# Kernel optimization log

Measured on AMD Instinct MI355X. Metric: run time of the kernel, lower is better.

## Reference

```python
import jax, jax.numpy as jnp
import numpy as np


def setup_inputs() -> dict:
    key = jax.random.key(0)
    k1, k2, k3, k4 = jax.random.split(key, 4)
    B, S, D_IN, D_OUT = 8, 2048, 4096, 4096
    inputs = jax.random.normal(k1, (B, S, D_IN), dtype=jnp.float32)
    # int8-valued weights stored as int32 (same math; original stores torch.int8)
    int8_weights = jax.random.randint(k2, (D_OUT, D_IN), -127, 128, dtype=jnp.int32)
    # realistic per-row dequant scales (small positive)
    scales = jax.random.uniform(k3, (D_OUT,), dtype=jnp.float32, minval=0.001, maxval=0.02)
    bias = jax.random.normal(k4, (1, D_OUT), dtype=jnp.float32) * 0.01
    return {"inputs": inputs, "int8_weights": int8_weights, "scales": scales, "bias": bias}


def reference(inputs, int8_weights, scales, bias):
    # converted_weights = int8_weights.to(inputs.dtype); F.linear(inputs, W) = inputs @ W.T
    w = int8_weights.astype(inputs.dtype)                      # [out, in]
    out = jnp.einsum('bsi,oi->bso', inputs, w)                 # [B, S, out]
    out = out * scales                                         # per-output-row scale
    out = out + bias                                           # bias broadcast [1, out]
    return out
```

## Files before the change

kernel.cpp:

```cpp
#include <hip/hip_runtime.h>
#include <hip/hip_bf16.h>

#define M_TOTAL 16384
#define N_TOTAL 4096
#define K_TOTAL 4096
#define NT (K_TOTAL / 128)

typedef __attribute__((ext_vector_type(4))) int i32x4;
typedef __attribute__((ext_vector_type(4))) float f32x4;

__device__ __forceinline__ unsigned pack4(int a, int b, int c, int d) {
  return (a & 0xFF) | ((b & 0xFF) << 8) | ((c & 0xFF) << 16) | ((d & 0xFF) << 24);
}

__global__ __launch_bounds__(256) void quant_a(const float* __restrict__ A,
                                               unsigned* __restrict__ Aq,
                                               float* __restrict__ ascale) {
  const int row = blockIdx.x;
  const int tid = threadIdx.x;
  const float4* src = reinterpret_cast<const float4*>(A + (size_t)row * K_TOTAL);
  float4 v[4];
#pragma unroll
  for (int c = 0; c < 4; ++c) v[c] = src[tid + 256 * c];
  float amax = 0.0f;
#pragma unroll
  for (int c = 0; c < 4; ++c) {
    amax = fmaxf(amax, fmaxf(fmaxf(fabsf(v[c].x), fabsf(v[c].y)),
                             fmaxf(fabsf(v[c].z), fabsf(v[c].w))));
  }
#pragma unroll
  for (int off = 32; off > 0; off >>= 1) amax = fmaxf(amax, __shfl_xor(amax, off, 64));
  __shared__ float wmax[4];
  if ((tid & 63) == 0) wmax[tid >> 6] = amax;
  __syncthreads();
  amax = fmaxf(fmaxf(wmax[0], wmax[1]), fmaxf(wmax[2], wmax[3]));
  amax = fmaxf(amax, 1e-20f);
  const float rs = 127.0f / amax;
  if (tid == 0) ascale[row] = amax * (1.0f / 127.0f);

  unsigned* dst = Aq + (size_t)row * (K_TOTAL / 4);
#pragma unroll
  for (int c = 0; c < 4; ++c) {
    int q[4];
    float f[4] = {v[c].x, v[c].y, v[c].z, v[c].w};
#pragma unroll
    for (int i = 0; i < 4; ++i) {
      int t = (int)rintf(f[i] * rs);
      q[i] = t < -127 ? -127 : (t > 127 ? 127 : t);
    }
    dst[tid + 256 * c] = pack4(q[0], q[1], q[2], q[3]);
  }
}

__global__ void cvt_w_i8(const int* __restrict__ W, unsigned* __restrict__ Wq, int n4) {
  const int stride = gridDim.x * blockDim.x;
  for (int i = blockIdx.x * blockDim.x + threadIdx.x; i < n4; i += stride) {
    int4 v = reinterpret_cast<const int4*>(W)[i];
    Wq[i] = pack4(v.x, v.y, v.z, v.w);
  }
}

#define GLOAD_LDS16(gp, lp)                                                \
  __builtin_amdgcn_global_load_lds(                                        \
      (const __attribute__((address_space(1))) void*)(gp),                 \
      (__attribute__((address_space(3))) void*)(lp), 16, 0, 0)

#define BAR() asm volatile("s_barrier" ::: "memory")
#define VM(n) asm volatile("s_waitcnt vmcnt(" #n ")" ::: "memory")


__global__ __launch_bounds__(512, 2) void w8a16_gemm_i8(
    const signed char* __restrict__ A,
    const signed char* __restrict__ Bt,
    const float* __restrict__ ascale,
    const float* __restrict__ scales, const float* __restrict__ bias,
    float* __restrict__ C) {
  __shared__ alignas(16) unsigned char lds[131072];

  const int tid = threadIdx.x;
  const int w = tid >> 6, l = tid & 63;
  const int wr = w >> 2, wc = w & 3;

  const int bid = blockIdx.x;
  const int swz = ((bid & 7) << 7) + (bid >> 3);
  const int bn = swz & 15, bm = swz >> 4;

  const int rowq = tid >> 3;
  const int colb = ((l & 7) ^ (l >> 3)) << 4;
  const signed char* pA = A + (size_t)(bm * 256 + rowq) * K_TOTAL + colb;
  const signed char* pB = Bt + (size_t)(bn * 256 + rowq) * K_TOTAL + colb;
  unsigned char* const ldsp = lds;
  const int woff = w << 10;

#define SDA(b_, h_) (ldsp + (b_) * 65536 + (h_) * 16384 + woff)
#define SDB(b_, h_) (ldsp + (b_) * 65536 + 32768 + (h_) * 16384 + woff)
#define STAGE_A(b_, h_, t_)                                                    \
  do {                                                                         \
    GLOAD_LDS16(pA + (size_t)((h_) * 128) * K_TOTAL + (t_) * 128, SDA(b_, h_));\
    GLOAD_LDS16(pA + (size_t)((h_) * 128 + 64) * K_TOTAL + (t_) * 128,         \
                SDA(b_, h_) + 8192);                                           \
  } while (0)
#define STAGE_B(b_, h_, t_)                                                    \
  do {                                                                         \
    GLOAD_LDS16(pB + (size_t)((h_) * 128) * K_TOTAL + (t_) * 128, SDB(b_, h_));\
    GLOAD_LDS16(pB + (size_t)((h_) * 128 + 64) * K_TOTAL + (t_) * 128,         \
                SDB(b_, h_) + 8192);                                           \
  } while (0)

  const int arow = ((l & 15) << 7) + ((((l >> 4) ^ (l & 7)) & 7) << 4);

  i32x4 af[8];
  i32x4 bfr[8];
  i32x4 acc[8][4] = {{}};

#define RD_A(mh_)                                                             \
  do {                                                                        \
    const unsigned char* Ab_ = ldsp + bsel * 65536 + wr * 16384;              \
    _Pragma("unroll") for (int fm = 0; fm < 4; ++fm)                          \
        _Pragma("unroll") for (int kk = 0; kk < 2; ++kk)                      \
            af[fm * 2 + kk] = *(const i32x4*)(Ab_ + ((mh_) * 4 + fm) * 2048 + \
                                              (arow ^ (kk << 6)));            \
  } while (0)
#define RD_B(nh_)                                                             \
  do {                                                                        \
    const unsigned char* Bb_ = ldsp + bsel * 65536 + 32768 +                  \
                               (wc >> 1) * 16384 + (wc & 1) * 8192;           \
    _Pragma("unroll") for (int fn = 0; fn < 2; ++fn)                          \
        _Pragma("unroll") for (int kk = 0; kk < 2; ++kk)                      \
            bfr[((nh_) * 2 + fn) * 2 + kk] =                                  \
                *(const i32x4*)(Bb_ + ((nh_) * 2 + fn) * 2048 +               \
                                (arow ^ (kk << 6)));                          \
  } while (0)
#define QUAD(mh_, nh_)                                                        \
  do {                                                                        \
    __builtin_amdgcn_s_setprio(1);                                            \
    _Pragma("unroll") for (int m = 0; m < 4; ++m)                             \
        _Pragma("unroll") for (int n = 0; n < 2; ++n)                         \
            _Pragma("unroll") for (int kk = 0; kk < 2; ++kk)                  \
                acc[(mh_) * 4 + m][(nh_) * 2 + n] =                           \
                    __builtin_amdgcn_mfma_i32_16x16x64_i8(                    \
                        af[m * 2 + kk], bfr[((nh_) * 2 + n) * 2 + kk],        \
                        acc[(mh_) * 4 + m][(nh_) * 2 + n], 0, 0, 0);          \
    __builtin_amdgcn_s_setprio(0);                                            \
  } while (0)

  STAGE_A(0, 0, 0); STAGE_A(0, 1, 0);
  STAGE_B(0, 0, 0); STAGE_B(0, 1, 0);
  STAGE_B(1, 0, 1); STAGE_B(1, 1, 1);
  STAGE_A(1, 0, 1);
  VM(6);
  BAR();

  for (int t = 0; t < NT; ++t) {
    const int bsel = t & 1;
    RD_A(0); RD_B(0);
    if (t + 1 < NT) STAGE_A(bsel ^ 1, 1, t + 1);
    BAR();
    QUAD(0, 0);
    BAR();
    RD_B(1);
    if (t + 2 < NT) STAGE_B(bsel, 0, t + 2);
    BAR();
    QUAD(0, 1);
    BAR();
    RD_A(1);
    if (t + 2 < NT) STAGE_B(bsel, 1, t + 2);
    BAR();
    QUAD(1, 1);
    BAR();
    if (t + 2 < NT) STAGE_A(bsel, 0, t + 2);
    BAR();
    QUAD(1, 0);
    if (t < NT - 2) { VM(6); } else { VM(0); }
    BAR();
  }

  const int row0 = bm * 256 + wr * 128 + ((l >> 4) << 2);
  const int col0 = bn * 256 + wc * 64 + (l & 15);
#pragma unroll
  for (int fn = 0; fn < 4; ++fn) {
    const int col = col0 + fn * 16;
    const float sc = scales[col];
    const float bi = bias[col];
#pragma unroll
    for (int fm = 0; fm < 8; ++fm) {
      const int r = row0 + fm * 16;
      float* cp = C + (size_t)r * N_TOTAL + col;
#pragma unroll
      for (int j = 0; j < 4; ++j)
        cp[(size_t)j * N_TOTAL] = fmaf((float)acc[fm][fn][j], ascale[r + j] * sc, bi);
    }
  }
}

__global__ void naive_gemm(const float* __restrict__ A, const int* __restrict__ W,
                           const float* __restrict__ scales, const float* __restrict__ bias,
                           float* __restrict__ C) {
  size_t idx = (size_t)blockIdx.x * blockDim.x + threadIdx.x;
  if (idx >= (size_t)M_TOTAL * N_TOTAL) return;
  const int n = (int)(idx % N_TOTAL);
  const size_t m = idx / N_TOTAL;
  const float* a = A + m * (size_t)K_TOTAL;
  const int* w = W + (size_t)n * K_TOTAL;
  float s = 0.f;
  for (int k = 0; k < K_TOTAL; ++k) s = fmaf(a[k], (float)w[k], s);
  C[idx] = fmaf(s, scales[n], bias[n]);
}

extern "C" void kernel_launch(void* const* d_in, const int* in_sizes, int n_in,
                              void* d_out, int out_size, void* d_ws, size_t ws_size,
                              hipStream_t stream) {
  const float* A = (const float*)d_in[0];
  const int* W = (const int*)d_in[1];
  const float* scales = (const float*)d_in[2];
  const float* bias = (const float*)d_in[3];
  float* out = (float*)d_out;

  const size_t a_elems = (size_t)M_TOTAL * K_TOTAL;
  const size_t w_elems = (size_t)N_TOTAL * K_TOTAL;
  const size_t need = a_elems + w_elems + (size_t)M_TOTAL * sizeof(float);

  if (ws_size >= need) {
    signed char* A_q = (signed char*)d_ws;
    signed char* W_q = A_q + a_elems;
    float* a_s = (float*)(W_q + w_elems);
    quant_a<<<M_TOTAL, 256, 0, stream>>>(A, (unsigned*)A_q, a_s);
    cvt_w_i8<<<2048, 256, 0, stream>>>(W, (unsigned*)W_q, (int)(w_elems / 4));
    w8a16_gemm_i8<<<1024, 512, 0, stream>>>(A_q, W_q, a_s, scales, bias, out);
  } else {
    size_t total = (size_t)M_TOTAL * N_TOTAL;
    naive_gemm<<<(unsigned)((total + 255) / 256), 256, 0, stream>>>(A, W, scales, bias, out);
  }
}
```

Baseline: 380.9 us.

## Load B fragments directly from global into registers, bypassing LDS

The weight (B) tile no longer goes through LDS. Each wave loads its own B fragments straight from global memory into registers, issued at the end of each k-step for the next step. A alone stays double-buffered in LDS, so shared memory use is halved, which may let more blocks fit per CU. The cost is losing B reuse across the two wave rows, which doubles B global/L2 traffic, and leaving little latency hiding for the register loads.

```diff
diff --git a/kernel.cpp b/kernel.cpp
--- a/kernel.cpp
+++ b/kernel.cpp
@@ -75,7 +75,7 @@
     const float* __restrict__ ascale,
     const float* __restrict__ scales, const float* __restrict__ bias,
     float* __restrict__ C) {
-  __shared__ alignas(16) unsigned char lds[131072];
+  __shared__ alignas(16) unsigned char lds[65536];
 
   const int tid = threadIdx.x;
   const int w = tid >> 6, l = tid & 63;
@@ -88,50 +88,45 @@
   const int rowq = tid >> 3;
   const int colb = ((l & 7) ^ (l >> 3)) << 4;
   const signed char* pA = A + (size_t)(bm * 256 + rowq) * K_TOTAL + colb;
-  const signed char* pB = Bt + (size_t)(bn * 256 + rowq) * K_TOTAL + colb;
   unsigned char* const ldsp = lds;
   const int woff = w << 10;
 
-#define SDA(b_, h_) (ldsp + (b_) * 65536 + (h_) * 16384 + woff)
-#define SDB(b_, h_) (ldsp + (b_) * 65536 + 32768 + (h_) * 16384 + woff)
+#define SDA(b_, h_) (ldsp + (b_) * 32768 + (h_) * 16384 + woff)
 #define STAGE_A(b_, h_, t_)                                                    \
   do {                                                                         \
     GLOAD_LDS16(pA + (size_t)((h_) * 128) * K_TOTAL + (t_) * 128, SDA(b_, h_));\
     GLOAD_LDS16(pA + (size_t)((h_) * 128 + 64) * K_TOTAL + (t_) * 128,         \
                 SDA(b_, h_) + 8192);                                           \
   } while (0)
-#define STAGE_B(b_, h_, t_)                                                    \
-  do {                                                                         \
-    GLOAD_LDS16(pB + (size_t)((h_) * 128) * K_TOTAL + (t_) * 128, SDB(b_, h_));\
-    GLOAD_LDS16(pB + (size_t)((h_) * 128 + 64) * K_TOTAL + (t_) * 128,         \
-                SDB(b_, h_) + 8192);                                           \
-  } while (0)
 
   const int arow = ((l & 15) << 7) + ((((l >> 4) ^ (l & 7)) & 7) << 4);
 
+  const signed char* pBg =
+      Bt + (size_t)(bn * 256 + wc * 64 + (l & 15)) * K_TOTAL + ((l >> 4) << 4);
+
   i32x4 af[8];
-  i32x4 bfr[8];
+  i32x4 b0[4], b1[4];
   i32x4 acc[8][4] = {{}};
 
 #define RD_A(mh_)                                                             \
   do {                                                                        \
-    const unsigned char* Ab_ = ldsp + bsel * 65536 + wr * 16384;              \
+    const unsigned char* Ab_ = ldsp + bsel * 32768 + wr * 16384;              \
     _Pragma("unroll") for (int fm = 0; fm < 4; ++fm)                          \
         _Pragma("unroll") for (int kk = 0; kk < 2; ++kk)                      \
             af[fm * 2 + kk] = *(const i32x4*)(Ab_ + ((mh_) * 4 + fm) * 2048 + \
                                               (arow ^ (kk << 6)));            \
   } while (0)
-#define RD_B(nh_)                                                             \
+#define ISSUE_B(t_)                                                           \
   do {                                                                        \
-    const unsigned char* Bb_ = ldsp + bsel * 65536 + 32768 +                  \
-                               (wc >> 1) * 16384 + (wc & 1) * 8192;           \
     _Pragma("unroll") for (int fn = 0; fn < 2; ++fn)                          \
-        _Pragma("unroll") for (int kk = 0; kk < 2; ++kk)                      \
-            bfr[((nh_) * 2 + fn) * 2 + kk] =                                  \
-                *(const i32x4*)(Bb_ + ((nh_) * 2 + fn) * 2048 +               \
-                                (arow ^ (kk << 6)));                          \
-  } while (0)
-#define QUAD(mh_, nh_)                                                        \
+        _Pragma("unroll") for (int kk = 0; kk < 2; ++kk) {                    \
+      b0[fn * 2 + kk] = *(const i32x4*)(pBg + (size_t)(fn * 16) * K_TOTAL +   \
+                                        (t_) * 128 + kk * 64);                \
+      b1[fn * 2 + kk] = *(const i32x4*)(pBg + (size_t)(32 + fn * 16) *        \
+                                            K_TOTAL + (t_) * 128 + kk * 64);  \
+    }                                                                         \
+  } while (0)
+#define QUAD(mh_, nh_, BF_)                                                   \
   do {                                                                        \
     __builtin_amdgcn_s_setprio(1);                                            \
     _Pragma("unroll") for (int m = 0; m < 4; ++m)                             \
@@ -139,39 +134,35 @@
             _Pragma("unroll") for (int kk = 0; kk < 2; ++kk)                  \
                 acc[(mh_) * 4 + m][(nh_) * 2 + n] =                           \
                     __builtin_amdgcn_mfma_i32_16x16x64_i8(                    \
-                        af[m * 2 + kk], bfr[((nh_) * 2 + n) * 2 + kk],        \
+                        af[m * 2 + kk], BF_[n * 2 + kk],                      \
                         acc[(mh_) * 4 + m][(nh_) * 2 + n], 0, 0, 0);          \
     __builtin_amdgcn_s_setprio(0);                                            \
   } while (0)
 
   STAGE_A(0, 0, 0); STAGE_A(0, 1, 0);
-  STAGE_B(0, 0, 0); STAGE_B(0, 1, 0);
-  STAGE_B(1, 0, 1); STAGE_B(1, 1, 1);
-  STAGE_A(1, 0, 1);
-  VM(6);
+  ISSUE_B(0);
+  VM(8);
   BAR();
 
   for (int t = 0; t < NT; ++t) {
     const int bsel = t & 1;
-    RD_A(0); RD_B(0);
+    RD_A(0);
+    if (t + 1 < NT) STAGE_A(bsel ^ 1, 0, t + 1);
+    BAR();
+    QUAD(0, 0, b0);
+    BAR();
     if (t + 1 < NT) STAGE_A(bsel ^ 1, 1, t + 1);
     BAR();
-    QUAD(0, 0);
-    BAR();
-    RD_B(1);
-    if (t + 2 < NT) STAGE_B(bsel, 0, t + 2);
-    BAR();
-    QUAD(0, 1);
+    QUAD(0, 1, b1);
     BAR();
     RD_A(1);
-    if (t + 2 < NT) STAGE_B(bsel, 1, t + 2);
-    BAR();
-    QUAD(1, 1);
-    BAR();
-    if (t + 2 < NT) STAGE_A(bsel, 0, t + 2);
-    BAR();
-    QUAD(1, 0);
-    if (t < NT - 2) { VM(6); } else { VM(0); }
+    BAR();
+    QUAD(1, 1, b1);
+    BAR();
+    BAR();
+    QUAD(1, 0, b0);
+    if (t + 1 < NT) ISSUE_B(t + 1);
+    if (t < NT - 1) { VM(8); }
     BAR();
   }
 
```

Measured after the change: 569.4 us. +49.5%, slower.

## Software-pipeline LDS fragment reads across K-tiles with double-buffered registers

Applied to the files above, without the earlier changes.

Restructures the int8 GEMM main loop so that the last MFMA quadrant of each K-tile is deferred into the next iteration. This lets the LDS reads for the next tile overlap with that quadrant's MFMAs, using separate A/B fragment register sets and a loop unrolled by two to alternate buffers. It also groups the three global->LDS stages together and adds sched_barriers to pin the instruction order. The extra fragment registers raise VGPR pressure under launch_bounds(512,2), which may cause spills, and the buffer-reuse timing has to stay correct across the barriers.

```diff
diff --git a/kernel.cpp b/kernel.cpp
--- a/kernel.cpp
+++ b/kernel.cpp
@@ -7,7 +7,6 @@
 #define NT (K_TOTAL / 128)
 
 typedef __attribute__((ext_vector_type(4))) int i32x4;
-typedef __attribute__((ext_vector_type(4))) float f32x4;
 
 __device__ __forceinline__ unsigned pack4(int a, int b, int c, int d) {
   return (a & 0xFF) | ((b & 0xFF) << 8) | ((c & 0xFF) << 16) | ((d & 0xFF) << 24);
@@ -24,10 +23,9 @@
   for (int c = 0; c < 4; ++c) v[c] = src[tid + 256 * c];
   float amax = 0.0f;
 #pragma unroll
-  for (int c = 0; c < 4; ++c) {
+  for (int c = 0; c < 4; ++c)
     amax = fmaxf(amax, fmaxf(fmaxf(fabsf(v[c].x), fabsf(v[c].y)),
                              fmaxf(fabsf(v[c].z), fabsf(v[c].w))));
-  }
 #pragma unroll
   for (int off = 32; off > 0; off >>= 1) amax = fmaxf(amax, __shfl_xor(amax, off, 64));
   __shared__ float wmax[4];
@@ -67,6 +65,7 @@
 
 #define BAR() asm volatile("s_barrier" ::: "memory")
 #define VM(n) asm volatile("s_waitcnt vmcnt(" #n ")" ::: "memory")
+#define SCHED0() __builtin_amdgcn_sched_barrier(0)
 
 
 __global__ __launch_bounds__(512, 2) void w8a16_gemm_i8(
@@ -108,30 +107,29 @@
   } while (0)
 
   const int arow = ((l & 15) << 7) + ((((l >> 4) ^ (l & 7)) & 7) << 4);
-
-  i32x4 af[8];
-  i32x4 bfr[8];
+  const int bOffC = 32768 + (wc >> 1) * 16384 + (wc & 1) * 8192;
+
+  i32x4 af0[8], af1[8];
+  i32x4 b0E[4], b0O[4], b1[4];
   i32x4 acc[8][4] = {{}};
 
-#define RD_A(mh_)                                                             \
-  do {                                                                        \
-    const unsigned char* Ab_ = ldsp + bsel * 65536 + wr * 16384;              \
+#define RD_AF(dst_, mh_, bsel_)                                               \
+  do {                                                                        \
+    const unsigned char* Ab_ = ldsp + (bsel_) * 65536 + wr * 16384;           \
     _Pragma("unroll") for (int fm = 0; fm < 4; ++fm)                          \
         _Pragma("unroll") for (int kk = 0; kk < 2; ++kk)                      \
-            af[fm * 2 + kk] = *(const i32x4*)(Ab_ + ((mh_) * 4 + fm) * 2048 + \
-                                              (arow ^ (kk << 6)));            \
-  } while (0)
-#define RD_B(nh_)                                                             \
-  do {                                                                        \
-    const unsigned char* Bb_ = ldsp + bsel * 65536 + 32768 +                  \
-                               (wc >> 1) * 16384 + (wc & 1) * 8192;           \
+            dst_[fm * 2 + kk] = *(const i32x4*)(                              \
+                Ab_ + ((mh_) * 4 + fm) * 2048 + (arow ^ (kk << 6)));          \
+  } while (0)
+#define RD_BH(dst_, nh_, bsel_)                                               \
+  do {                                                                        \
+    const unsigned char* Bb_ = ldsp + (bsel_) * 65536 + bOffC;                \
     _Pragma("unroll") for (int fn = 0; fn < 2; ++fn)                          \
         _Pragma("unroll") for (int kk = 0; kk < 2; ++kk)                      \
-            bfr[((nh_) * 2 + fn) * 2 + kk] =                                  \
-                *(const i32x4*)(Bb_ + ((nh_) * 2 + fn) * 2048 +               \
-                                (arow ^ (kk << 6)));                          \
-  } while (0)
-#define QUAD(mh_, nh_)                                                        \
+            dst_[fn * 2 + kk] = *(const i32x4*)(                              \
+                Bb_ + ((nh_) * 2 + fn) * 2048 + (arow ^ (kk << 6)));          \
+  } while (0)
+#define QUAD(mh_, nh_, AF_, BF_)                                              \
   do {                                                                        \
     __builtin_amdgcn_s_setprio(1);                                            \
     _Pragma("unroll") for (int m = 0; m < 4; ++m)                             \
@@ -139,41 +137,51 @@
             _Pragma("unroll") for (int kk = 0; kk < 2; ++kk)                  \
                 acc[(mh_) * 4 + m][(nh_) * 2 + n] =                           \
                     __builtin_amdgcn_mfma_i32_16x16x64_i8(                    \
-                        af[m * 2 + kk], bfr[((nh_) * 2 + n) * 2 + kk],        \
+                        AF_[m * 2 + kk], BF_[n * 2 + kk],                     \
                         acc[(mh_) * 4 + m][(nh_) * 2 + n], 0, 0, 0);          \
     __builtin_amdgcn_s_setprio(0);                                            \
   } while (0)
 
-  STAGE_A(0, 0, 0); STAGE_A(0, 1, 0);
-  STAGE_B(0, 0, 0); STAGE_B(0, 1, 0);
-  STAGE_B(1, 0, 1); STAGE_B(1, 1, 1);
-  STAGE_A(1, 0, 1);
+#define TILE_BODY(t_, bsel_, BNEW_, BPREV_, doprev_)                          \
+  do {                                                                        \
+                                                                      \
+    RD_AF(af0, 0, bsel_);                                                     \
+    RD_BH(BNEW_, 0, bsel_);                                                   \
+    if ((t_) + 1 < NT) STAGE_A((bsel_) ^ 1, 1, (t_) + 1);                     \
+    SCHED0(); BAR();                                                          \
+    if (doprev_) QUAD(1, 0, af1, BPREV_);                                     \
+    SCHED0(); BAR();                                                          \
+                                                                      \
+    RD_AF(af1, 1, bsel_);                                                     \
+    RD_BH(b1, 1, bsel_);                                                      \
+    SCHED0(); BAR();                                                          \
+    QUAD(0, 0, af0, BNEW_);                                                   \
+    SCHED0(); BAR();                                                          \
+                                                                      \
+    QUAD(0, 1, af0, b1);                                                      \
+    SCHED0(); BAR();                                                          \
+                                                                      \
+    if ((t_) + 2 < NT) {                                                      \
+      STAGE_B(bsel_, 0, (t_) + 2);                                            \
+      STAGE_B(bsel_, 1, (t_) + 2);                                            \
+      STAGE_A(bsel_, 0, (t_) + 2);                                            \
+    }                                                                         \
+    SCHED0(); BAR();                                                          \
+    QUAD(1, 1, af1, b1);                                                      \
+    if ((t_) < NT - 2) { VM(6); } else { VM(0); }                             \
+    SCHED0(); BAR();                                                          \
+  } while (0)
+
+  STAGE_A(0, 0, 0); STAGE_A(0, 1, 0); STAGE_B(0, 0, 0); STAGE_B(0, 1, 0);
+  STAGE_B(1, 0, 1); STAGE_B(1, 1, 1); STAGE_A(1, 0, 1);
   VM(6);
   BAR();
 
-  for (int t = 0; t < NT; ++t) {
-    const int bsel = t & 1;
-    RD_A(0); RD_B(0);
-    if (t + 1 < NT) STAGE_A(bsel ^ 1, 1, t + 1);
-    BAR();
-    QUAD(0, 0);
-    BAR();
-    RD_B(1);
-    if (t + 2 < NT) STAGE_B(bsel, 0, t + 2);
-    BAR();
-    QUAD(0, 1);
-    BAR();
-    RD_A(1);
-    if (t + 2 < NT) STAGE_B(bsel, 1, t + 2);
-    BAR();
-    QUAD(1, 1);
-    BAR();
-    if (t + 2 < NT) STAGE_A(bsel, 0, t + 2);
-    BAR();
-    QUAD(1, 0);
-    if (t < NT - 2) { VM(6); } else { VM(0); }
-    BAR();
-  }
+  for (int tt = 0; tt < NT; tt += 2) {
+    TILE_BODY(tt, 0, b0E, b0O, (tt > 0));
+    TILE_BODY(tt + 1, 1, b0O, b0E, 1);
+  }
+  QUAD(1, 0, af1, b0O);
 
   const int row0 = bm * 256 + wr * 128 + ((l >> 4) << 2);
   const int col0 = bn * 256 + wc * 64 + (l & 15);
```

After: 414.6 us. +8.8%, slower.

## Fuse weight and activation quantization kernels and restructure GEMM prefetch schedule

Applied to the files above, without the earlier changes.

Merges the weight int8 packing and the activation quantization into a single launch, splitting work by block index, to remove one kernel launch and its tail. In the GEMM main loop, both A halves are prefetched one tile ahead and both B halves two tiles ahead together. Pairs of MFMA quads are run between fewer barriers. This cuts synchronization count but shortens A's prefetch distance and changes load/compute overlap.

```diff
diff --git a/kernel.cpp b/kernel.cpp
--- a/kernel.cpp
+++ b/kernel.cpp
@@ -5,29 +5,38 @@
 #define N_TOTAL 4096
 #define K_TOTAL 4096
 #define NT (K_TOTAL / 128)
+#define W_BLOCKS 2048
 
 typedef __attribute__((ext_vector_type(4))) int i32x4;
-typedef __attribute__((ext_vector_type(4))) float f32x4;
 
 __device__ __forceinline__ unsigned pack4(int a, int b, int c, int d) {
   return (a & 0xFF) | ((b & 0xFF) << 8) | ((c & 0xFF) << 16) | ((d & 0xFF) << 24);
 }
 
-__global__ __launch_bounds__(256) void quant_a(const float* __restrict__ A,
-                                               unsigned* __restrict__ Aq,
-                                               float* __restrict__ ascale) {
-  const int row = blockIdx.x;
+__global__ __launch_bounds__(256) void cvt_fused(
+    const float* __restrict__ A, unsigned* __restrict__ Aq,
+    float* __restrict__ ascale, const int* __restrict__ W,
+    unsigned* __restrict__ Wq) {
   const int tid = threadIdx.x;
+  if (blockIdx.x < W_BLOCKS) {
+    const int n4 = (N_TOTAL * K_TOTAL) / 4;
+    const int stride = W_BLOCKS * 256;
+    for (int i = blockIdx.x * 256 + tid; i < n4; i += stride) {
+      int4 v = reinterpret_cast<const int4*>(W)[i];
+      Wq[i] = pack4(v.x, v.y, v.z, v.w);
+    }
+    return;
+  }
+  const int row = blockIdx.x - W_BLOCKS;
   const float4* src = reinterpret_cast<const float4*>(A + (size_t)row * K_TOTAL);
   float4 v[4];
 #pragma unroll
   for (int c = 0; c < 4; ++c) v[c] = src[tid + 256 * c];
   float amax = 0.0f;
 #pragma unroll
-  for (int c = 0; c < 4; ++c) {
+  for (int c = 0; c < 4; ++c)
     amax = fmaxf(amax, fmaxf(fmaxf(fabsf(v[c].x), fabsf(v[c].y)),
                              fmaxf(fabsf(v[c].z), fabsf(v[c].w))));
-  }
 #pragma unroll
   for (int off = 32; off > 0; off >>= 1) amax = fmaxf(amax, __shfl_xor(amax, off, 64));
   __shared__ float wmax[4];
@@ -49,14 +58,6 @@
       q[i] = t < -127 ? -127 : (t > 127 ? 127 : t);
     }
     dst[tid + 256 * c] = pack4(q[0], q[1], q[2], q[3]);
-  }
-}
-
-__global__ void cvt_w_i8(const int* __restrict__ W, unsigned* __restrict__ Wq, int n4) {
-  const int stride = gridDim.x * blockDim.x;
-  for (int i = blockIdx.x * blockDim.x + threadIdx.x; i < n4; i += stride) {
-    int4 v = reinterpret_cast<const int4*>(W)[i];
-    Wq[i] = pack4(v.x, v.y, v.z, v.w);
   }
 }
 
@@ -147,31 +148,24 @@
   STAGE_A(0, 0, 0); STAGE_A(0, 1, 0);
   STAGE_B(0, 0, 0); STAGE_B(0, 1, 0);
   STAGE_B(1, 0, 1); STAGE_B(1, 1, 1);
-  STAGE_A(1, 0, 1);
-  VM(6);
+  VM(4);
   BAR();
 
   for (int t = 0; t < NT; ++t) {
     const int bsel = t & 1;
-    RD_A(0); RD_B(0);
-    if (t + 1 < NT) STAGE_A(bsel ^ 1, 1, t + 1);
+    RD_A(0);
+    RD_B(0); RD_B(1);
+    if (t + 1 < NT) { STAGE_A(bsel ^ 1, 0, t + 1); STAGE_A(bsel ^ 1, 1, t + 1); }
     BAR();
     QUAD(0, 0);
-    BAR();
-    RD_B(1);
-    if (t + 2 < NT) STAGE_B(bsel, 0, t + 2);
-    BAR();
     QUAD(0, 1);
     BAR();
     RD_A(1);
-    if (t + 2 < NT) STAGE_B(bsel, 1, t + 2);
+    if (t + 2 < NT) { STAGE_B(bsel, 0, t + 2); STAGE_B(bsel, 1, t + 2); }
     BAR();
     QUAD(1, 1);
-    BAR();
-    if (t + 2 < NT) STAGE_A(bsel, 0, t + 2);
-    BAR();
     QUAD(1, 0);
-    if (t < NT - 2) { VM(6); } else { VM(0); }
+    if (t < NT - 2) { VM(4); } else { VM(0); }
     BAR();
   }
 
@@ -224,8 +218,8 @@
     signed char* A_q = (signed char*)d_ws;
     signed char* W_q = A_q + a_elems;
     float* a_s = (float*)(W_q + w_elems);
-    quant_a<<<M_TOTAL, 256, 0, stream>>>(A, (unsigned*)A_q, a_s);
-    cvt_w_i8<<<2048, 256, 0, stream>>>(W, (unsigned*)W_q, (int)(w_elems / 4));
+    cvt_fused<<<W_BLOCKS + M_TOTAL, 256, 0, stream>>>(A, (unsigned*)A_q, a_s, W,
+                                                      (unsigned*)W_q);
     w8a16_gemm_i8<<<1024, 512, 0, stream>>>(A_q, W_q, a_s, scales, bias, out);
   } else {
     size_t total = (size_t)M_TOTAL * N_TOTAL;
```

Measured after the change: 378.5 us. Within noise of the previous version (-0.7%).
